# Kernel tuning notes

Measured on AMD Instinct MI355X. Metric: run time of the kernel, lower is better.

## Reference

```python
import jax, jax.numpy as jnp
import numpy as np

EMBED_DIM = 1024
NUM_HEADS = 16
HEAD_DIM = EMBED_DIM // NUM_HEADS
LN_EPS = 1e-5


def setup_inputs() -> dict:
    key = jax.random.key(0)
    ks = jax.random.split(key, 12)
    B, SQ, SKV, E = 2, 1024, 4096, EMBED_DIM
    s = 1.0 / np.sqrt(E)
    return {
        "query": jax.random.normal(ks[0], (B, SQ, E), jnp.float32),
        "key_value": jax.random.normal(ks[1], (B, SKV, E), jnp.float32),
        "key_value_mask": jax.random.randint(ks[2], (B, SKV), 0, 2, jnp.int32),
        "Wq": jax.random.normal(ks[3], (E, E), jnp.float32) * s,
        "bq": jnp.zeros((E,), jnp.float32),
        "Wk": jax.random.normal(ks[4], (E, E), jnp.float32) * s,
        "bk": jnp.zeros((E,), jnp.float32),
        "Wv": jax.random.normal(ks[5], (E, E), jnp.float32) * s,
        "bv": jnp.zeros((E,), jnp.float32),
        "Wo": jax.random.normal(ks[6], (E, E), jnp.float32) * s,
        "bo": jnp.zeros((E,), jnp.float32),
        "ln_gamma": jnp.ones((E,), jnp.float32),
        "ln_beta": jnp.zeros((E,), jnp.float32),
    }


def reference(query, key_value, key_value_mask, Wq, bq, Wk, bk, Wv, bv, Wo, bo, ln_gamma, ln_beta):
    B, SQ, E = query.shape
    SKV = key_value.shape[1]
    H, D = NUM_HEADS, HEAD_DIM
    # projections (dropout is eval-mode identity)
    q = (query @ Wq.T + bq).reshape(B, SQ, H, D).transpose(0, 2, 1, 3)      # b h sq d
    k = (key_value @ Wk.T + bk).reshape(B, SKV, H, D).transpose(0, 2, 1, 3)  # b h skv d
    v = (key_value @ Wv.T + bv).reshape(B, SKV, H, D).transpose(0, 2, 1, 3)
    scale = jnp.sqrt(jnp.asarray(D, q.dtype))
    scores = jnp.einsum('bhqd,bhkd->bhqk', q, k) / scale                     # b h sq skv
    mask = (key_value_mask != 0)[:, None, None, :]                           # b 1 1 skv
    scores = jnp.where(mask, scores, jnp.asarray(-jnp.inf, scores.dtype))
    attn = jax.nn.softmax(scores, axis=-1)
    out = jnp.einsum('bhqk,bhkd->bhqd', attn, v)
    out = out.transpose(0, 2, 1, 3).reshape(B, SQ, E)
    out = out @ Wo.T + bo
    # post-LN residual
    x = query + out
    mu = jnp.mean(x, axis=-1, keepdims=True)
    var = jnp.mean(jnp.square(x - mu), axis=-1, keepdims=True)
    return (x - mu) * jax.lax.rsqrt(var + LN_EPS) * ln_gamma + ln_beta
```

## Files before the change

### kernel.cpp

```cpp
#include <hip/hip_runtime.h>
#include <cstdint>


typedef __bf16 bf16x8_t  __attribute__((ext_vector_type(8)));
typedef float  f32x4_t   __attribute__((ext_vector_type(4)));
typedef float  f32x16_t  __attribute__((ext_vector_type(16)));

#define E_DIM 1024
#define NH    16
#define HD    64
#define SCALE_L2E 0.1803368804f

__device__ __forceinline__ unsigned short f32_bf16(float f) {
    union { float f; unsigned int u; } v; v.f = f;
    unsigned int u = v.u;
    unsigned int r = (u + 0x7fffu + ((u >> 16) & 1u)) >> 16;
    return (unsigned short)r;
}

__device__ __forceinline__ unsigned pack_bf16(float a, float b) {
    __bf16 x = (__bf16)a, y = (__bf16)b;
    unsigned short ux = __builtin_bit_cast(unsigned short, x);
    unsigned short uy = __builtin_bit_cast(unsigned short, y);
    return (unsigned)ux | ((unsigned)uy << 16);
}

__device__ __forceinline__ void gld16(const unsigned short* g, unsigned short* l) {
    __builtin_amdgcn_global_load_lds(
        (const __attribute__((address_space(1))) unsigned int*)g,
        (__attribute__((address_space(3))) unsigned int*)l, 16, 0, 0);
}

__device__ __forceinline__ bf16x8_t ld16g(const unsigned short* p) {
    union { uint4 u; bf16x8_t f; } v;
    v.u = *reinterpret_cast<const uint4*>(p);
    return v.f;
}

__global__ void cast_all(const float* __restrict__ q, const float* __restrict__ kv,
                         const float* __restrict__ wq, const float* __restrict__ wk,
                         const float* __restrict__ wv, const float* __restrict__ wo,
                         unsigned short* __restrict__ Xq, unsigned short* __restrict__ Xkv,
                         unsigned short* __restrict__ Wqb, unsigned short* __restrict__ Wkb,
                         unsigned short* __restrict__ Wvb, unsigned short* __restrict__ Wob,
                         const int* __restrict__ msk, float* __restrict__ Sub) {
    __shared__ int red[4];
    if (blockIdx.x >= 14336) {
        int b = blockIdx.x - 14336, t = threadIdx.x;
        int s = 0;
#pragma unroll
        for (int k = 0; k < 16; k++) s += (msk[b * 4096 + k * 256 + t] != 0);
#pragma unroll
        for (int off = 32; off >= 1; off >>= 1) s += __shfl_xor(s, off, 64);
        if ((t & 63) == 0) red[t >> 6] = s;
        __syncthreads();
        if (t == 0)
            Sub[b] = (float)(4096 - (red[0] + red[1] + red[2] + red[3]));
        return;
    }
    long i = (long)blockIdx.x * 256 + threadIdx.x;
    const float* src; unsigned short* dst; long off;
    if (i < 2621440) {
        if (i < 524288) { src = q;  dst = Xq;  off = i; }
        else            { src = kv; dst = Xkv; off = i - 524288; }
    } else {
        long j = i - 2621440;
        int w = (int)(j >> 18); off = j & 262143;
        src = (w == 0) ? wq : (w == 1) ? wk : (w == 2) ? wv : wo;
        dst = (w == 0) ? Wqb : (w == 1) ? Wkb : (w == 2) ? Wvb : Wob;
    }
    float4 v = reinterpret_cast<const float4*>(src)[off];
    ushort4 o;
    o.x = f32_bf16(v.x); o.y = f32_bf16(v.y);
    o.z = f32_bf16(v.z); o.w = f32_bf16(v.w);
    reinterpret_cast<ushort4*>(dst)[off] = o;
}

#define BK 64

__global__ __launch_bounds__(256) void gemm_qkv(
    const unsigned short* __restrict__ Xq,
    const unsigned short* __restrict__ Xkv,
    const unsigned short* __restrict__ Wqb,
    const unsigned short* __restrict__ Wkb,
    const unsigned short* __restrict__ Wvb,
    const float* __restrict__ bq,
    const float* __restrict__ bk,
    const float* __restrict__ bv,
    unsigned short* __restrict__ Qout,
    unsigned short* __restrict__ Kout,
    unsigned short* __restrict__ Vout,
    const int* __restrict__ kvm)
{
    __shared__ __align__(16) unsigned short As[128 * BK];
    __shared__ __align__(16) unsigned short Bs[128 * BK];
    int bid  = blockIdx.x;
    int tid  = threadIdx.x;
    int lane = tid & 63;
    int wvu  = __builtin_amdgcn_readfirstlane(tid >> 6);
    int l15  = lane & 15, quad = lane >> 4, x7 = l15 & 7;

    if (bid < 1024) {
        int bx   = bid & 15;
        int isV  = bx >= 8;
        int m0   = (bid >> 4) * 128;
        int n0   = (bx & 7) * 128;
        const unsigned short* W = isV ? Wvb : Wkb;
        const float* bias = isV ? bv : bk;
        int wm   = ((tid >> 6) >> 1) * 64, wn = ((tid >> 6) & 1) * 64;

        f32x4_t acc[4][4];
#pragma unroll
        for (int i = 0; i < 4; i++)
#pragma unroll
            for (int j = 0; j < 4; j++) acc[i][j] = (f32x4_t)(0.f);

        for (int k0 = 0; k0 < 1024; k0 += BK) {
            __syncthreads();
#pragma unroll
            for (int i = 0; i < 4; i++) {
                int s = (i * 4 + wvu) * 64 + lane;
                int row = s >> 3, pcol = ((s & 7) ^ (row & 7)) << 3;
                gld16(&Xkv[(long)(m0 + row) * 1024 + k0 + pcol], &As[(i * 4 + wvu) * 512]);
                gld16(&W[(long)(n0 + row) * 1024 + k0 + pcol], &Bs[(i * 4 + wvu) * 512]);
            }
            __syncthreads();
            const char* Ab = (const char*)As;
            const char* Bb = (const char*)Bs;
#pragma unroll
            for (int ks = 0; ks < 2; ks++) {
                int pos = (((ks << 2) + quad) ^ x7) << 4;
                bf16x8_t af[4], bf[4];
#pragma unroll
                for (int mi = 0; mi < 4; mi++)
                    af[mi] = *reinterpret_cast<const bf16x8_t*>(
                        Ab + (wm + mi * 16 + l15) * 128 + pos);
#pragma unroll
                for (int ni = 0; ni < 4; ni++)
                    bf[ni] = *reinterpret_cast<const bf16x8_t*>(
                        Bb + (wn + ni * 16 + l15) * 128 + pos);
#pragma unroll
                for (int mi = 0; mi < 4; mi++)
#pragma unroll
                    for (int ni = 0; ni < 4; ni++)
                        acc[mi][ni] = __builtin_amdgcn_mfma_f32_16x16x32_bf16(
                            af[mi], bf[ni], acc[mi][ni], 0, 0, 0);
            }
        }
        int4 mk[4];
#pragma unroll
        for (int mi = 0; mi < 4; mi++) {
            int mg0 = m0 + wm + mi * 16 + quad * 4;
            mk[mi] = *reinterpret_cast<const int4*>(&kvm[mg0]);
        }
        if (!isV) {
#pragma unroll
            for (int mi = 0; mi < 4; mi++)
#pragma unroll
                for (int ni = 0; ni < 4; ni++) {
                    int n = n0 + wn + ni * 16 + l15;
                    float bvv = bias[n];
                    int h = n >> 6, d = n & 63;
#pragma unroll
                    for (int r = 0; r < 4; r++) {
                        int mg = m0 + wm + mi * 16 + quad * 4 + r;
                        int b = mg >> 12, s = mg & 4095;
                        unsigned short val = (&mk[mi].x)[r]
                            ? f32_bf16(acc[mi][ni][r] + bvv) : (unsigned short)0;
                        Kout[(((b * NH + h) << 12) + s) * HD + d] = val;
                    }
                }
        } else {
#pragma unroll
            for (int mi = 0; mi < 4; mi++)
#pragma unroll
                for (int ni = 0; ni < 4; ni++) {
                    int n = n0 + wn + ni * 16 + l15;
                    float bvv = bias[n];
                    int h = n >> 6, d = n & 63;
                    int mg0 = m0 + wm + mi * 16 + quad * 4;
                    int b = mg0 >> 12, s = mg0 & 4095;
                    ushort4 w;
                    w.x = mk[mi].x ? f32_bf16(acc[mi][ni][0] + bvv) : (unsigned short)0;
                    w.y = mk[mi].y ? f32_bf16(acc[mi][ni][1] + bvv) : (unsigned short)0;
                    w.z = mk[mi].z ? f32_bf16(acc[mi][ni][2] + bvv) : (unsigned short)0;
                    w.w = mk[mi].w ? f32_bf16(acc[mi][ni][3] + bvv) : (unsigned short)0;
                    *reinterpret_cast<ushort4*>(
                        &Vout[(((b * NH + h) * HD + d) << 12) + s]) = w;
                }
        }
    } else {
        int t    = bid - 1024;
        int m0   = (t >> 3) * 64;
        int n0   = (t & 7) * 128;
        int wm   = ((tid >> 6) >> 1) * 32, wn = ((tid >> 6) & 1) * 64;

        f32x4_t acc[2][4];
#pragma unroll
        for (int i = 0; i < 2; i++)
#pragma unroll
            for (int j = 0; j < 4; j++) acc[i][j] = (f32x4_t)(0.f);

        for (int k0 = 0; k0 < 1024; k0 += BK) {
            __syncthreads();
#pragma unroll
            for (int i = 0; i < 2; i++) {
                int s = (i * 4 + wvu) * 64 + lane;
                int row = s >> 3, pcol = ((s & 7) ^ (row & 7)) << 3;
                gld16(&Xq[(long)(m0 + row) * 1024 + k0 + pcol], &As[(i * 4 + wvu) * 512]);
            }
#pragma unroll
            for (int i = 0; i < 4; i++) {
                int s = (i * 4 + wvu) * 64 + lane;
                int row = s >> 3, pcol = ((s & 7) ^ (row & 7)) << 3;
                gld16(&Wqb[(long)(n0 + row) * 1024 + k0 + pcol], &Bs[(i * 4 + wvu) * 512]);
            }
            __syncthreads();
            const char* Ab = (const char*)As;
            const char* Bb = (const char*)Bs;
#pragma unroll
            for (int ks = 0; ks < 2; ks++) {
                int pos = (((ks << 2) + quad) ^ x7) << 4;
                bf16x8_t af[2], bf[4];
#pragma unroll
                for (int mi = 0; mi < 2; mi++)
                    af[mi] = *reinterpret_cast<const bf16x8_t*>(
                        Ab + (wm + mi * 16 + l15) * 128 + pos);
#pragma unroll
                for (int ni = 0; ni < 4; ni++)
                    bf[ni] = *reinterpret_cast<const bf16x8_t*>(
                        Bb + (wn + ni * 16 + l15) * 128 + pos);
#pragma unroll
                for (int mi = 0; mi < 2; mi++)
#pragma unroll
                    for (int ni = 0; ni < 4; ni++)
                        acc[mi][ni] = __builtin_amdgcn_mfma_f32_16x16x32_bf16(
                            af[mi], bf[ni], acc[mi][ni], 0, 0, 0);
            }
        }
#pragma unroll
        for (int mi = 0; mi < 2; mi++)
#pragma unroll
            for (int ni = 0; ni < 4; ni++) {
                int n = n0 + wn + ni * 16 + l15;
                float bvq = bq[n];
                int h = n >> 6, d = n & 63;
#pragma unroll
                for (int r = 0; r < 4; r++) {
                    int mg = m0 + wm + mi * 16 + quad * 4 + r;
                    int b = mg >> 10, s = mg & 1023;
                    Qout[(((b * NH + h) << 10) + s) * HD + d] =
                        f32_bf16((acc[mi][ni][r] + bvq) * SCALE_L2E);
                }
            }
    }
}

__global__ __launch_bounds__(256) void gemm_oproj(
    const unsigned short* __restrict__ A,
    const unsigned short* __restrict__ W,
    const float* __restrict__ bias,
    const float* __restrict__ resid,
    float* __restrict__ xout)
{
    __shared__ __align__(16) unsigned short As[32 * BK];
    __shared__ __align__(16) unsigned short Bs[64 * BK];
    int tid  = threadIdx.x;
    int m0   = blockIdx.y * 32;
    int n0   = blockIdx.x * 64;
    int lane = tid & 63;
    int wvu  = __builtin_amdgcn_readfirstlane(tid >> 6);
    int l15  = lane & 15, quad = lane >> 4, x7 = l15 & 7;
    int wn   = (tid >> 6) * 16;

    f32x4_t acc[2];
    acc[0] = (f32x4_t)(0.f); acc[1] = (f32x4_t)(0.f);

    for (int k0 = 0; k0 < 1024; k0 += BK) {
        __syncthreads();
        {
            int s = wvu * 64 + lane;
            int row = s >> 3, pcol = ((s & 7) ^ (row & 7)) << 3;
            gld16(&A[(long)(m0 + row) * 1024 + k0 + pcol], &As[wvu * 512]);
        }
#pragma unroll
        for (int i = 0; i < 2; i++) {
            int s = (i * 4 + wvu) * 64 + lane;
            int row = s >> 3, pcol = ((s & 7) ^ (row & 7)) << 3;
            gld16(&W[(long)(n0 + row) * 1024 + k0 + pcol], &Bs[(i * 4 + wvu) * 512]);
        }
        __syncthreads();
        const char* Ab = (const char*)As;
        const char* Bb = (const char*)Bs;
#pragma unroll
        for (int ks = 0; ks < 2; ks++) {
            int pos = (((ks << 2) + quad) ^ x7) << 4;
            bf16x8_t af[2], bf;
#pragma unroll
            for (int mi = 0; mi < 2; mi++)
                af[mi] = *reinterpret_cast<const bf16x8_t*>(
                    Ab + (mi * 16 + l15) * 128 + pos);
            bf = *reinterpret_cast<const bf16x8_t*>(
                Bb + (wn + l15) * 128 + pos);
#pragma unroll
            for (int mi = 0; mi < 2; mi++)
                acc[mi] = __builtin_amdgcn_mfma_f32_16x16x32_bf16(
                    af[mi], bf, acc[mi], 0, 0, 0);
        }
    }
    int n = n0 + wn + l15;
    float bv = bias[n];
#pragma unroll
    for (int mi = 0; mi < 2; mi++)
#pragma unroll
        for (int r = 0; r < 4; r++) {
            int mg = m0 + mi * 16 + quad * 4 + r;
            xout[mg * 1024 + n] = acc[mi][r] + bv + resid[mg * 1024 + n];
        }
}

__global__ __launch_bounds__(512, 4) void attn_kernel(
    const unsigned short* __restrict__ Q,
    const unsigned short* __restrict__ K,
    const unsigned short* __restrict__ VT,
    float* __restrict__ Osc,
    float* __restrict__ Lsc)
{
    __shared__ __align__(16) union {
        struct { unsigned short Kb[2][4096]; unsigned short Vb[2][4096]; } st;
        struct { float OL[4][2048]; float ls[128]; } mg;
    } sm;

    int tid  = threadIdx.x;
    int lane = tid & 63;
    int w    = tid >> 6;
    int wvu  = __builtin_amdgcn_readfirstlane(w);
    int l31  = lane & 31, hw = lane >> 5;
    int qsub = w & 3, kvsub = w >> 2;

    int bid  = blockIdx.x;
    int xcd  = bid & 7, gidx = bid >> 3;
    int bh   = xcd * 4 + (gidx & 3);
    int rest = gidx >> 2;
    int q0   = (rest & 7) * 128;
    int bhalf = rest >> 3;

    const unsigned short* Kb = K + ((long)bh * 4096 + bhalf * 2048) * HD;
    const unsigned short* Vb = VT + (long)bh * HD * 4096 + bhalf * 2048;
    const unsigned short* Qb = Q + ((long)bh * 1024 + q0) * HD;

    bf16x8_t qfr[4];
#pragma unroll
    for (int ks = 0; ks < 4; ks++)
        qfr[ks] = ld16g(Qb + (qsub * 32 + l31) * HD + ks * 16 + hw * 8);

    f32x16_t oacc[2];
    oacc[0] = (f32x16_t)(0.f); oacc[1] = (f32x16_t)(0.f);
    float l_run = 0.f;

    auto stage = [&](int kt, int bufi) {
        int s = wvu * 64 + lane;
        int row = s >> 3, pc = ((s & 7) ^ (row & 7)) << 3;
        gld16(&Kb[(long)(kt * 64 + row) * HD + pc], &sm.st.Kb[bufi][wvu * 512]);
        gld16(&Vb[(long)row * 4096 + kt * 64 + pc], &sm.st.Vb[bufi][wvu * 512]);
    };

    const char* Kc = (const char*)sm.st.Kb;
    const char* Vc = (const char*)sm.st.Vb;

    stage(0, 0);
#pragma unroll 2
    for (int kt = 0; kt < 32; kt++) {
        __syncthreads();
        if (kt + 1 < 32) stage(kt + 1, (kt + 1) & 1);
        int bo = (kt & 1) * 8192;

        f32x16_t sa = (f32x16_t)(0.f);
        int krow = kvsub * 32 + l31;
        __builtin_amdgcn_s_setprio(1);
#pragma unroll
        for (int ks = 0; ks < 4; ks++) {
            int phys = (ks * 2 + hw) ^ (krow & 7);
            bf16x8_t kf = *reinterpret_cast<const bf16x8_t*>(
                Kc + bo + krow * 128 + phys * 16);
            sa = __builtin_amdgcn_mfma_f32_32x32x16_bf16(kf, qfr[ks], sa, 0, 0, 0);
        }
        __builtin_amdgcn_s_setprio(0);

        float pv[16];
#pragma unroll
        for (int r = 0; r < 16; r++) pv[r] = exp2f(sa[r]);
        float s0 = (pv[0] + pv[1]) + (pv[2] + pv[3]);
        float s1 = (pv[4] + pv[5]) + (pv[6] + pv[7]);
        float s2 = (pv[8] + pv[9]) + (pv[10] + pv[11]);
        float s3 = (pv[12] + pv[13]) + (pv[14] + pv[15]);
        l_run += (s0 + s1) + (s2 + s3);
        unsigned pku[8];
#pragma unroll
        for (int s4 = 0; s4 < 4; s4++) {
            pku[s4 * 2 + 0] = pack_bf16(pv[s4 * 4 + 0], pv[s4 * 4 + 1]);
            pku[s4 * 2 + 1] = pack_bf16(pv[s4 * 4 + 2], pv[s4 * 4 + 3]);
        }

        __builtin_amdgcn_s_setprio(1);
#pragma unroll
        for (int ks2 = 0; ks2 < 2; ks2++) {
            unsigned x0 = pku[(ks2 * 2) * 2 + 0];
            unsigned x1 = pku[(ks2 * 2) * 2 + 1];
            unsigned z0 = pku[(ks2 * 2 + 1) * 2 + 0];
            unsigned z1 = pku[(ks2 * 2 + 1) * 2 + 1];
            asm("v_permlane32_swap_b32 %0, %1" : "+v"(x0), "+v"(z0));
            asm("v_permlane32_swap_b32 %0, %1" : "+v"(x1), "+v"(z1));
            union { uint4 u; bf16x8_t f; } bw;
            bw.u.x = x0; bw.u.y = x1; bw.u.z = z0; bw.u.w = z1;
            int c = kvsub * 4 + ks2 * 2 + hw;
#pragma unroll
            for (int ds = 0; ds < 2; ds++) {
                int vrow = ds * 32 + l31;
                int phys = c ^ (vrow & 7);
                bf16x8_t va = *reinterpret_cast<const bf16x8_t*>(
                    Vc + bo + vrow * 128 + phys * 16);
                oacc[ds] = __builtin_amdgcn_mfma_f32_32x32x16_bf16(
                    va, bw.f, oacc[ds], 0, 0, 0);
            }
        }
        __builtin_amdgcn_s_setprio(0);
    }

    l_run += __shfl_xor(l_run, 32, 64);
    __syncthreads();
    if (kvsub == 1) {
        float* OL = sm.mg.OL[qsub];
#pragma unroll
        for (int ds = 0; ds < 2; ds++)
#pragma unroll
            for (int r = 0; r < 16; r++) {
                int d = ds * 32 + (r & 3) + 8 * (r >> 2) + 4 * hw;
                OL[d * 32 + l31] = oacc[ds][r];
            }
        if (hw == 0) sm.mg.ls[qsub * 32 + l31] = l_run;
    }
    __syncthreads();
    if (kvsub == 0) {
        const float* OL = sm.mg.OL[qsub];
        int q = q0 + qsub * 32 + l31;
        long obase = (((long)bhalf * 32 + bh) * 64) * 1024;
#pragma unroll
        for (int ds = 0; ds < 2; ds++)
#pragma unroll
            for (int r = 0; r < 16; r++) {
                int d = ds * 32 + (r & 3) + 8 * (r >> 2) + 4 * hw;
                Osc[obase + (long)d * 1024 + q] = oacc[ds][r] + OL[d * 32 + l31];
            }
        if (hw == 0)
            Lsc[((long)bhalf * 32 + bh) * 1024 + q] = l_run + sm.mg.ls[qsub * 32 + l31];
    }
}

__global__ __launch_bounds__(256) void attn_merge(
    const float* __restrict__ Osc, const float* __restrict__ Lsc,
    const float* __restrict__ Sub, unsigned short* __restrict__ AO)
{
    __shared__ unsigned short T[64 * 66];
    int t = threadIdx.x, w = t >> 6, lane = t & 63;
    int bh = blockIdx.y, b = bh >> 4, h = bh & 15;
    int q0 = blockIdx.x * 64;
    int q = q0 + lane;

    float ls = Lsc[(long)bh * 1024 + q]
             + Lsc[(long)(32 + bh) * 1024 + q] - Sub[b];
    float inv = __builtin_amdgcn_rcpf(ls);
    inv = inv * (2.f - ls * inv);

#pragma unroll
    for (int dd = 0; dd < 16; dd++) {
        int d = w * 16 + dd;
        long base = (long)bh * 64 * 1024 + (long)d * 1024 + q;
        float o = Osc[base] + Osc[base + 32l * 64 * 1024];
        T[lane * 66 + d] = f32_bf16(o * inv);
    }
    __syncthreads();
    int q2 = t >> 2, c16 = (t & 3) * 16;
    unsigned ov[8];
#pragma unroll
    for (int j = 0; j < 8; j++)
        ov[j] = *reinterpret_cast<const unsigned*>(&T[q2 * 66 + c16 + j * 2]);
    unsigned short* dst = &AO[((long)(b * 1024 + q0 + q2)) * E_DIM + h * HD + c16];
    reinterpret_cast<uint4*>(dst)[0] = make_uint4(ov[0], ov[1], ov[2], ov[3]);
    reinterpret_cast<uint4*>(dst)[1] = make_uint4(ov[4], ov[5], ov[6], ov[7]);
}

__global__ __launch_bounds__(256) void ln_kernel(
    const float* __restrict__ x, const float* __restrict__ g,
    const float* __restrict__ be, float* __restrict__ out)
{
    __shared__ float red[8];
    int row = blockIdx.x, tid = threadIdx.x;
    float4 v = reinterpret_cast<const float4*>(x)[row * 256 + tid];
    float s  = v.x + v.y + v.z + v.w;
    float sq = v.x * v.x + v.y * v.y + v.z * v.z + v.w * v.w;
#pragma unroll
    for (int off = 32; off >= 1; off >>= 1) {
        s  += __shfl_xor(s,  off, 64);
        sq += __shfl_xor(sq, off, 64);
    }
    if ((tid & 63) == 0) { red[tid >> 6] = s; red[4 + (tid >> 6)] = sq; }
    __syncthreads();
    s  = red[0] + red[1] + red[2] + red[3];
    sq = red[4] + red[5] + red[6] + red[7];
    float mu  = s * (1.f / 1024.f);
    float var = sq * (1.f / 1024.f) - mu * mu;
    float rs  = rsqrtf(var + 1e-5f);
    int c = tid * 4;
    float4 o;
    o.x = (v.x - mu) * rs * g[c]     + be[c];
    o.y = (v.y - mu) * rs * g[c + 1] + be[c + 1];
    o.z = (v.z - mu) * rs * g[c + 2] + be[c + 2];
    o.w = (v.w - mu) * rs * g[c + 3] + be[c + 3];
    reinterpret_cast<float4*>(out)[row * 256 + tid] = o;
}

extern "C" void kernel_launch(void* const* d_in, const int* in_sizes, int n_in,
                              void* d_out, int out_size, void* d_ws, size_t ws_size,
                              hipStream_t stream) {
    const float* query     = (const float*)d_in[0];
    const float* key_value = (const float*)d_in[1];
    const int*   kv_mask   = (const int*)d_in[2];
    const float* Wq = (const float*)d_in[3];
    const float* bq = (const float*)d_in[4];
    const float* Wk = (const float*)d_in[5];
    const float* bk = (const float*)d_in[6];
    const float* Wv = (const float*)d_in[7];
    const float* bv = (const float*)d_in[8];
    const float* Wo = (const float*)d_in[9];
    const float* bo = (const float*)d_in[10];
    const float* ln_g = (const float*)d_in[11];
    const float* ln_b = (const float*)d_in[12];
    float* out = (float*)d_out;

    char* ws = (char*)d_ws;
    unsigned short* Xq  = (unsigned short*)(ws);
    unsigned short* Xkv = (unsigned short*)(ws + (4ll  << 20));
    unsigned short* Wqb = (unsigned short*)(ws + (20ll << 20));
    unsigned short* Wkb = (unsigned short*)(ws + (22ll << 20));
    unsigned short* Wvb = (unsigned short*)(ws + (24ll << 20));
    float*          Osc = (float*)(ws);
    unsigned short* Kh  = (unsigned short*)(ws + (32ll << 20));
    unsigned short* VTh = (unsigned short*)(ws + (48ll << 20));
    unsigned short* AO  = (unsigned short*)(ws + (64ll << 20));
    float*          Xr  = (float*)(ws + (68ll << 20));
    float*          Lsc = (float*)(ws + (76ll << 20));
    float*          Sub = (float*)(ws + (77ll << 20));
    unsigned short* Qh  = (unsigned short*)(ws + (80ll << 20));
    unsigned short* Wob = (unsigned short*)(ws + (84ll << 20));

    cast_all<<<14338, 256, 0, stream>>>(query, key_value, Wq, Wk, Wv, Wo,
                                        Xq, Xkv, Wqb, Wkb, Wvb, Wob,
                                        kv_mask, Sub);

    gemm_qkv<<<1280, 256, 0, stream>>>(Xq, Xkv, Wqb, Wkb, Wvb, bq, bk, bv,
                                       Qh, Kh, VTh, kv_mask);

    attn_kernel<<<512, 512, 0, stream>>>(Qh, Kh, VTh, Osc, Lsc);
    attn_merge<<<dim3(16, 32), 256, 0, stream>>>(Osc, Lsc, Sub, AO);

    gemm_oproj<<<dim3(16, 64), 256, 0, stream>>>(AO, Wob, bo, query, Xr);

    ln_kernel<<<2048, 256, 0, stream>>>(Xr, ln_g, ln_b, out);
}
```

Measured before the change: 249.7 us.

## Split attention KV range four ways and remap QKV GEMM blocks per XCD

The attention kernel now splits each head's 4096 keys into four 1024-key chunks instead of two. This doubles the grid to 1024 blocks and halves the loop length. The merge kernel sums four partial outputs and four partial denominators. Separately, the QKV projection GEMM maps block IDs so that consecutive blocks on one XCD share M tiles, which should improve L2 reuse. The attention launch-bounds occupancy hint is raised. The cost is twice the fp32 partial-output traffic through the merge step and a larger scratch buffer.

```diff
diff --git a/kernel.cpp b/kernel.cpp
--- a/kernel.cpp
+++ b/kernel.cpp
@@ -101,10 +101,13 @@
     int l15  = lane & 15, quad = lane >> 4, x7 = l15 & 7;
 
     if (bid < 1024) {
-        int bx   = bid & 15;
-        int isV  = bx >= 8;
-        int m0   = (bid >> 4) * 128;
-        int n0   = (bx & 7) * 128;
+        int xcd  = bid & 7;
+        int j    = bid >> 3;
+        int mt   = xcd * 8 + (j >> 4);
+        int sel  = j & 15;
+        int isV  = sel >= 8;
+        int m0   = mt * 128;
+        int n0   = (sel & 7) * 128;
         const unsigned short* W = isV ? Wvb : Wkb;
         const float* bias = isV ? bv : bk;
         int wm   = ((tid >> 6) >> 1) * 64, wn = ((tid >> 6) & 1) * 64;
@@ -113,7 +116,7 @@
 #pragma unroll
         for (int i = 0; i < 4; i++)
 #pragma unroll
-            for (int j = 0; j < 4; j++) acc[i][j] = (f32x4_t)(0.f);
+            for (int jj = 0; jj < 4; jj++) acc[i][jj] = (f32x4_t)(0.f);
 
         for (int k0 = 0; k0 < 1024; k0 += BK) {
             __syncthreads();
@@ -191,15 +194,18 @@
         }
     } else {
         int t    = bid - 1024;
-        int m0   = (t >> 3) * 64;
-        int n0   = (t & 7) * 128;
+        int xcd  = bid & 7;
+        int j    = t >> 3;
+        int mt   = xcd * 4 + (j >> 3);
+        int m0   = mt * 64;
+        int n0   = (j & 7) * 128;
         int wm   = ((tid >> 6) >> 1) * 32, wn = ((tid >> 6) & 1) * 64;
 
         f32x4_t acc[2][4];
 #pragma unroll
         for (int i = 0; i < 2; i++)
 #pragma unroll
-            for (int j = 0; j < 4; j++) acc[i][j] = (f32x4_t)(0.f);
+            for (int jj = 0; jj < 4; jj++) acc[i][jj] = (f32x4_t)(0.f);
 
         for (int k0 = 0; k0 < 1024; k0 += BK) {
             __syncthreads();
@@ -319,7 +325,7 @@
         }
 }
 
-__global__ __launch_bounds__(512, 4) void attn_kernel(
+__global__ __launch_bounds__(512, 8) void attn_kernel(
     const unsigned short* __restrict__ Q,
     const unsigned short* __restrict__ K,
     const unsigned short* __restrict__ VT,
@@ -343,10 +349,10 @@
     int bh   = xcd * 4 + (gidx & 3);
     int rest = gidx >> 2;
     int q0   = (rest & 7) * 128;
-    int bhalf = rest >> 3;
-
-    const unsigned short* Kb = K + ((long)bh * 4096 + bhalf * 2048) * HD;
-    const unsigned short* Vb = VT + (long)bh * HD * 4096 + bhalf * 2048;
+    int bq4  = rest >> 3;
+
+    const unsigned short* Kb = K + ((long)bh * 4096 + bq4 * 1024) * HD;
+    const unsigned short* Vb = VT + (long)bh * HD * 4096 + bq4 * 1024;
     const unsigned short* Qb = Q + ((long)bh * 1024 + q0) * HD;
 
     bf16x8_t qfr[4];
@@ -370,9 +376,9 @@
 
     stage(0, 0);
 #pragma unroll 2
-    for (int kt = 0; kt < 32; kt++) {
+    for (int kt = 0; kt < 16; kt++) {
         __syncthreads();
-        if (kt + 1 < 32) stage(kt + 1, (kt + 1) & 1);
+        if (kt + 1 < 16) stage(kt + 1, (kt + 1) & 1);
         int bo = (kt & 1) * 8192;
 
         f32x16_t sa = (f32x16_t)(0.f);
@@ -444,7 +450,7 @@
     if (kvsub == 0) {
         const float* OL = sm.mg.OL[qsub];
         int q = q0 + qsub * 32 + l31;
-        long obase = (((long)bhalf * 32 + bh) * 64) * 1024;
+        long obase = (((long)bq4 * 32 + bh) * 64) * 1024;
 #pragma unroll
         for (int ds = 0; ds < 2; ds++)
 #pragma unroll
@@ -453,7 +459,7 @@
                 Osc[obase + (long)d * 1024 + q] = oacc[ds][r] + OL[d * 32 + l31];
             }
         if (hw == 0)
-            Lsc[((long)bhalf * 32 + bh) * 1024 + q] = l_run + sm.mg.ls[qsub * 32 + l31];
+            Lsc[((long)bq4 * 32 + bh) * 1024 + q] = l_run + sm.mg.ls[qsub * 32 + l31];
     }
 }
 
@@ -467,8 +473,10 @@
     int q0 = blockIdx.x * 64;
     int q = q0 + lane;
 
-    float ls = Lsc[(long)bh * 1024 + q]
-             + Lsc[(long)(32 + bh) * 1024 + q] - Sub[b];
+    float ls = -Sub[b];
+#pragma unroll
+    for (int p = 0; p < 4; p++)
+        ls += Lsc[((long)(p * 32 + bh)) * 1024 + q];
     float inv = __builtin_amdgcn_rcpf(ls);
     inv = inv * (2.f - ls * inv);
 
@@ -476,7 +484,10 @@
     for (int dd = 0; dd < 16; dd++) {
         int d = w * 16 + dd;
         long base = (long)bh * 64 * 1024 + (long)d * 1024 + q;
-        float o = Osc[base] + Osc[base + 32l * 64 * 1024];
+        float o = 0.f;
+#pragma unroll
+        for (int p = 0; p < 4; p++)
+            o += Osc[base + (long)p * 32 * 64 * 1024];
         T[lane * 66 + d] = f32_bf16(o * inv);
     }
     __syncthreads();
@@ -561,7 +572,7 @@
     gemm_qkv<<<1280, 256, 0, stream>>>(Xq, Xkv, Wqb, Wkb, Wvb, bq, bk, bv,
                                        Qh, Kh, VTh, kv_mask);
 
-    attn_kernel<<<512, 512, 0, stream>>>(Qh, Kh, VTh, Osc, Lsc);
+    attn_kernel<<<1024, 512, 0, stream>>>(Qh, Kh, VTh, Osc, Lsc);
     attn_merge<<<dim3(16, 32), 256, 0, stream>>>(Osc, Lsc, Sub, AO);
 
     gemm_oproj<<<dim3(16, 64), 256, 0, stream>>>(AO, Wob, bo, query, Xr);
```

New measurement: 351.2 us. +40.7%, slower.
